# Performance work log

Measured on AMD Instinct MI355X. Metric: run time of the kernel, lower is better.

## Reference

```python
import jax, jax.numpy as jnp
import numpy as np

B, N, D = 2, 1024, 512
H, DH = 8, 64
HD = H * DH
FF = 2048
DEPTH = 4
SCALE = DH ** -0.5


def layer_norm(x, g, b, eps=1e-5):
    m = jnp.mean(x, axis=-1, keepdims=True)
    v = jnp.mean((x - m) ** 2, axis=-1, keepdims=True)
    return (x - m) / jnp.sqrt(v + eps) * g + b


def rel_shift(x):
    # x: (i, j, b, h) -> Transformer-XL relative shift via pad/reshape/slice
    i, j = x.shape[0], x.shape[1]
    zp = jnp.zeros((i, 1) + x.shape[2:], x.dtype)
    xp = jnp.concatenate([zp, x], axis=1).reshape((j + 1, i) + x.shape[2:])
    return xp[1:].reshape(x.shape)


def setup_inputs() -> dict:
    key = jax.random.key(0)
    ks = jax.random.split(key, 20)
    s = 0.02
    inp = {
        'x':   jax.random.normal(ks[0], (B, N, D), jnp.float32),
        'r_t': jax.random.normal(ks[1], (B, N, D), jnp.float32),
        'r_c': jax.random.normal(ks[2], (B, N, D), jnp.float32),
        'r_p': jax.random.normal(ks[3], (B, N, D), jnp.float32),
        'bias_pf': jax.random.normal(ks[4], (H, DH), jnp.float32) * s,
        'ln1_g': jnp.ones((DEPTH, D), jnp.float32),
        'ln1_b': jnp.zeros((DEPTH, D), jnp.float32),
        'w_qkv': jax.random.normal(ks[5], (DEPTH, D, 3 * HD), jnp.float32) * s,
        'w_out': jax.random.normal(ks[6], (DEPTH, HD, D), jnp.float32) * s,
        'b_out': jnp.zeros((DEPTH, D), jnp.float32),
        'w_kt': jax.random.normal(ks[7], (DEPTH, D, HD), jnp.float32) * s,
        'w_kc': jax.random.normal(ks[8], (DEPTH, D, HD), jnp.float32) * s,
        'w_kp': jax.random.normal(ks[9], (DEPTH, D, HD), jnp.float32) * s,
        'ln2_g': jnp.ones((DEPTH, D), jnp.float32),
        'ln2_b': jnp.zeros((DEPTH, D), jnp.float32),
        'w_ff1': jax.random.normal(ks[10], (DEPTH, D, FF), jnp.float32) * s,
        'b_ff1': jnp.zeros((DEPTH, FF), jnp.float32),
        'w_ff2': jax.random.normal(ks[11], (DEPTH, FF, D), jnp.float32) * s,
        'b_ff2': jnp.zeros((DEPTH, D), jnp.float32),
    }
    return inp


def _to_nbhd(t, b, n):
    # (b, n, h*d) -> (n, b, h, d)
    return t.reshape(b, n, H, DH).transpose(1, 0, 2, 3)


def reference(x, r_t, r_c, r_p, bias_pf, ln1_g, ln1_b, w_qkv, w_out, b_out,
              w_kt, w_kc, w_kp, ln2_g, ln2_b, w_ff1, b_ff1, w_ff2, b_ff2):
    b, n, _ = x.shape
    attn_last = None
    for l in range(DEPTH):
        xn = layer_norm(x, ln1_g[l], ln1_b[l])
        qkv = xn @ w_qkv[l]  # (b, n, 3*HD)
        q, k, v = jnp.split(qkv, 3, axis=-1)
        q = _to_nbhd(q, b, n) + bias_pf  # Ex_Wq + bias_pf, (n,b,h,d)
        k = _to_nbhd(k, b, n)
        v = _to_nbhd(v, b, n)
        wt = _to_nbhd(r_t @ w_kt[l], b, n)
        wc = _to_nbhd(r_c @ w_kc[l], b, n)
        wp = _to_nbhd(r_p @ w_kp[l], b, n)
        AC = jnp.einsum('ibhd,jbhd->ijbh', q, k)
        BD = (rel_shift(jnp.einsum('ibhd,jbhd->ijbh', q, wt))
              + rel_shift(jnp.einsum('ibhd,jbhd->ijbh', q, wc))
              + rel_shift(jnp.einsum('ibhd,jbhd->ijbh', q, wp))) * (1.0 / 3.0)
        dots = (AC + BD) * SCALE
        # NOTE: source uses nn.Softmax(dim=-1) on (i,j,b,h), i.e. over heads.
        attn = jax.nn.softmax(dots, axis=-1)
        out = jnp.einsum('ijbh,jbhd->ibhd', attn, v)
        out = out.transpose(1, 0, 2, 3).reshape(b, n, HD)
        x = out @ w_out[l] + b_out[l] + x
        xn2 = layer_norm(x, ln2_g[l], ln2_b[l])
        h1 = jax.nn.gelu(xn2 @ w_ff1[l] + b_ff1[l], approximate=False)
        x = h1 @ w_ff2[l] + b_ff2[l] + x
        attn_last = attn
    # attention rearranged 'q k b h -> b h q k'
    return x, attn_last.transpose(2, 3, 0, 1)
```

## Files before the change

### kernel.cpp

```cpp
#include <hip/hip_runtime.h>
#include <hip/hip_bf16.h>


using bf16 = __hip_bfloat16;
typedef __attribute__((ext_vector_type(8))) short short8;
typedef __attribute__((ext_vector_type(4))) float float4v;
typedef __attribute__((ext_vector_type(2))) unsigned int uint2v;

__device__ __forceinline__ float ldsel(const void* p, long long i, bool isbf) {
    return isbf ? __bfloat162float(((const bf16*)p)[i]) : ((const float*)p)[i];
}
__device__ __forceinline__ float bf2f(short u) {
    return __uint_as_float(((unsigned)(unsigned short)u) << 16);
}
__device__ __forceinline__ short f2bf(float f) {
    bf16 h = __float2bfloat16(f);
    return *reinterpret_cast<short*>(&h);
}

__global__ void detect_kernel(const unsigned int* __restrict__ g, int* __restrict__ flag) {
    if (threadIdx.x == 0) flag[0] = ((g[0] & 0xFFFFu) != 0u) ? 1 : 0;
}

__global__ __launch_bounds__(256) void input_prep(
    const void* __restrict__ x_in, const void* __restrict__ r0,
    const void* __restrict__ r1, const void* __restrict__ r2,
    float* __restrict__ xbuf, bf16* __restrict__ rcat,
    const int* __restrict__ flagp) {
    bool bf = flagp[0] != 0;
    int y = blockIdx.y;
    int i = blockIdx.x * 256 + threadIdx.x;
    if (y == 0) {
        long long b = (long long)i * 8;
        if (bf) {
            short8 v = *(const short8*)((const bf16*)x_in + b);
            float4v o0, o1;
            #pragma unroll
            for (int j = 0; j < 4; ++j) { o0[j] = bf2f(v[j]); o1[j] = bf2f(v[4 + j]); }
            *(float4v*)(xbuf + b) = o0;
            *(float4v*)(xbuf + b + 4) = o1;
        } else {
            float4v a0 = *(const float4v*)((const float*)x_in + b);
            float4v a1 = *(const float4v*)((const float*)x_in + b + 4);
            *(float4v*)(xbuf + b) = a0;
            *(float4v*)(xbuf + b + 4) = a1;
        }
    } else {
        int s = y - 1;
        const void* src = (s == 0) ? r0 : ((s == 1) ? r1 : r2);
        int m = i >> 6, k8 = (i & 63) * 8;
        long long b = (long long)m * 512 + k8;
        short8 v;
        if (bf) {
            v = *(const short8*)((const bf16*)src + b);
        } else {
            float4v a0 = *(const float4v*)((const float*)src + b);
            float4v a1 = *(const float4v*)((const float*)src + b + 4);
            #pragma unroll
            for (int j = 0; j < 4; ++j) { v[j] = f2bf(a0[j]); v[4 + j] = f2bf(a1[j]); }
        }
        *(short8*)(rcat + (size_t)m * 1536 + s * 512 + k8) = v;
    }
}

__global__ __launch_bounds__(256) void outputs_kernel(
    const float* __restrict__ xbuf, const bf16* __restrict__ attn,
    void* __restrict__ out, const int* __restrict__ flagp) {
    bool bf = flagp[0] != 0;
    int bid = blockIdx.x;
    if (bid < 512) {
        long long b = ((long long)bid * 256 + threadIdx.x) * 8;
        float4v a0 = *(const float4v*)(xbuf + b);
        float4v a1 = *(const float4v*)(xbuf + b + 4);
        if (bf) {
            short8 v;
            #pragma unroll
            for (int j = 0; j < 4; ++j) { v[j] = f2bf(a0[j]); v[4 + j] = f2bf(a1[j]); }
            *(short8*)((bf16*)out + b) = v;
        } else {
            *(float4v*)((float*)out + b) = a0;
            *(float4v*)((float*)out + b + 4) = a1;
        }
    } else {
        long long e = ((long long)(bid - 512) * 256 + threadIdx.x) * 8;
        short8 v = *(const short8*)(attn + e);
        if (bf) {
            *(short8*)((bf16*)out + 1048576 + e) = v;
        } else {
            float4v o0, o1;
            #pragma unroll
            for (int j = 0; j < 4; ++j) { o0[j] = bf2f(v[j]); o1[j] = bf2f(v[4 + j]); }
            float* op = (float*)out + 1048576 + e;
            *(float4v*)op = o0;
            *(float4v*)(op + 4) = o1;
        }
    }
}

__global__ __launch_bounds__(256) void prep_weights(
    const void* __restrict__ s0, const void* __restrict__ s1, const void* __restrict__ s2,
    const void* __restrict__ s3, const void* __restrict__ s4, const void* __restrict__ s5,
    const void* __restrict__ s6, const void* __restrict__ g1, const void* __restrict__ g2,
    bf16* __restrict__ arena, const int* __restrict__ flagp) {
    const bool bf = flagp[0] != 0;
    const int bid = blockIdx.x;
    const int l = bid / 960;
    const int rem = bid - l * 960;
    const int LW = 3932160;
    const int L = l * LW;

    int j, tile, tx, ldi, ldo;
    long long ioff;
    int dstoff;
    if (rem < 192)      { j = 0; tile = rem;                tx = 24; ldi = 1536; ldo = 512;
                          ioff = (long long)l * 786432;  dstoff = L; }
    else if (rem < 448) { j = 1 + ((rem - 192) >> 6); tile = (rem - 192) & 63; tx = 8; ldi = 512;
                          ioff = (long long)l * 262144;
                          if (j <= 3) { ldo = 1536; dstoff = L + 786432 + (j - 1) * 512; }
                          else        { ldo = 512;  dstoff = L + 1572864; } }
    else if (rem < 704) { j = 5; tile = rem - 448;          tx = 32; ldi = 2048; ldo = 512;
                          ioff = (long long)l * 1048576; dstoff = L + 1835008; }
    else                { j = 6; tile = rem - 704;          tx = 8;  ldi = 512;  ldo = 2048;
                          ioff = (long long)l * 1048576; dstoff = L + 2883584; }
    const void* in = (j == 0) ? s0 : (j == 1) ? s1 : (j == 2) ? s2 :
                     (j == 3) ? s3 : (j == 4) ? s4 : (j == 5) ? s5 : s6;
    const int gsel = (j == 0) ? 1 : ((j == 5) ? 2 : 0);
    bf16* out = arena + dstoff;
    const int bx = tile % tx, by = tile / tx;
    const int n0 = bx * 64, k0 = by * 64;
    const int tid = threadIdx.x;

    __shared__ bf16 t[64][72];

    if (bf) {
        const bf16* inb = (const bf16*)in + ioff;
        #pragma unroll
        for (int p = 0; p < 2; ++p) {
            int e = tid + p * 256;
            int r = e >> 3, c = (e & 7) * 8;
            *(uint4*)&t[r][c] = *(const uint4*)(inb + (size_t)(k0 + r) * ldi + n0 + c);
        }
    } else {
        const float* inf = (const float*)in + ioff;
        #pragma unroll
        for (int p = 0; p < 4; ++p) {
            int e = tid + p * 256;
            int r = e >> 4, c = (e & 15) * 4;
            float4v v = *(const float4v*)(inf + (size_t)(k0 + r) * ldi + n0 + c);
            union { bf16 h[4]; uint2v u; } w;
            #pragma unroll
            for (int q = 0; q < 4; ++q) w.h[q] = __float2bfloat16(v[q]);
            *reinterpret_cast<uint2v*>(&t[r][c]) = w.u;
        }
    }
    __syncthreads();
    #pragma unroll
    for (int p = 0; p < 2; ++p) {
        int e = tid + p * 256;
        int r = e >> 3, c = (e & 7) * 8;
        union { short8 s; uint4 u; } o;
        if (gsel) {
            const void* gp = (gsel == 1) ? g1 : g2;
            const long long go = (long long)l * 512 + k0 + c;
            #pragma unroll
            for (int q = 0; q < 8; ++q) {
                float gv = ldsel(gp, go + q, bf);
                o.s[q] = f2bf(bf2f(*reinterpret_cast<const short*>(&t[c + q][r])) * gv);
            }
        } else {
            #pragma unroll
            for (int q = 0; q < 8; ++q)
                o.s[q] = *reinterpret_cast<const short*>(&t[c + q][r]);
        }
        *(uint4*)(out + (size_t)(n0 + r) * ldo + k0 + c) = o.u;
    }
}

__global__ __launch_bounds__(256) void bvec_kernel(
    const void* __restrict__ w_qkv, const void* __restrict__ w_ff1,
    const void* __restrict__ ln1_b, const void* __restrict__ ln2_b,
    const void* __restrict__ bias_pf, const void* __restrict__ b_ff1,
    float* __restrict__ bBq, float* __restrict__ bBf,
    const int* __restrict__ flagp) {
    bool bf = flagp[0] != 0;
    int bid = blockIdx.x;
    int l = bid / 14, r = bid - l * 14;
    int tid = threadIdx.x;
    __shared__ float bs[512];

    const void* W; long long woff; int ldw, n0; const void* beta; float* out;
    if (r < 6) { W = w_qkv; woff = (long long)l * 786432;  ldw = 1536; n0 = r * 256;
                 beta = ln1_b; out = bBq + l * 1536; }
    else       { W = w_ff1; woff = (long long)l * 1048576; ldw = 2048; n0 = (r - 6) * 256;
                 beta = ln2_b; out = bBf + l * 2048; }
    long long boff = (long long)l * 512;
    bs[tid]       = ldsel(beta, boff + tid, bf);
    bs[tid + 256] = ldsel(beta, boff + tid + 256, bf);
    __syncthreads();
    float acc = 0.f;
    #pragma unroll 8
    for (int k = 0; k < 512; ++k)
        acc += bs[k] * ldsel(W, woff + (long long)k * ldw + n0 + tid, bf);
    int n = n0 + tid;
    if (r < 6) { if (n < 512) acc += ldsel(bias_pf, n, bf); }
    else       { acc += ldsel(b_ff1, (long long)l * 2048 + n, bf); }
    out[n] = acc;
}

__global__ __launch_bounds__(256) void ln_stats(const float* __restrict__ x,
                                                float2* __restrict__ st) {
    int row = blockIdx.x;
    const float* xr = x + (size_t)row * 512;
    int tid = threadIdx.x;
    float v0 = xr[tid], v1 = xr[tid + 256];
    float s = v0 + v1, q = v0 * v0 + v1 * v1;
    #pragma unroll
    for (int off = 32; off; off >>= 1) {
        s += __shfl_down(s, off);
        q += __shfl_down(q, off);
    }
    __shared__ float ls[4], lq[4];
    int wid = tid >> 6, lane = tid & 63;
    if (lane == 0) { ls[wid] = s; lq[wid] = q; }
    __syncthreads();
    if (tid == 0) {
        float ts = ls[0] + ls[1] + ls[2] + ls[3];
        float tq = lq[0] + lq[1] + lq[2] + lq[3];
        float m = ts * (1.f / 512.f);
        float var = tq * (1.f / 512.f) - m * m;
        st[row] = make_float2(m, rsqrtf(var + 1e-5f));
    }
}

template<int EPI>
__global__ __launch_bounds__(256) void mgemm64(
    const bf16* __restrict__ A, int lda, long long sAb, long long sAh,
    const bf16* __restrict__ B, int ldb, long long sBb, long long sBh,
    void* __restrict__ Cv, int ldc, long long sCb, long long sCh,
    int K,
    const void* __restrict__ bias, long long biasoff,
    float* __restrict__ resid,
    const int* __restrict__ flagp) {
    const bool flg = flagp[0] != 0;
    const int tid = threadIdx.x;
    const int lane = tid & 63, wave = tid >> 6;
    const int m0 = blockIdx.y * 64, n0 = blockIdx.x * 64;
    const int zb = (int)(blockIdx.z >> 3), zh = (int)(blockIdx.z & 7);
    A += (size_t)zb * sAb + (size_t)zh * sAh;
    B += (size_t)zb * sBb + (size_t)zh * sBh;

    __shared__ bf16 As[64][40];
    __shared__ bf16 Bs[64][40];

    const int ar = tid >> 2, ak = (tid & 3) * 8;
    const bf16* Ap = A + (size_t)(m0 + ar) * lda + ak;
    const bf16* Bp = B + (size_t)(n0 + ar) * ldb + ak;

    const int wm = (wave >> 1) * 32, wn = (wave & 1) * 32;
    const int fr = lane & 15, fq = lane >> 4;

    float4v acc[2][2] = {};

    uint4 a0 = *(const uint4*)Ap;
    uint4 b0 = *(const uint4*)Bp;

    for (int k0 = 0; k0 < K; k0 += 32) {
        __syncthreads();
        *(uint4*)&As[ar][ak] = a0;
        *(uint4*)&Bs[ar][ak] = b0;
        if (k0 + 32 < K) {
            a0 = *(const uint4*)(Ap + k0 + 32);
            b0 = *(const uint4*)(Bp + k0 + 32);
        }
        __syncthreads();
        union { uint4 u; short8 s; } ua[2], ub[2];
        #pragma unroll
        for (int i = 0; i < 2; ++i) ua[i].u = *(const uint4*)&As[wm + i * 16 + fr][fq * 8];
        #pragma unroll
        for (int j = 0; j < 2; ++j) ub[j].u = *(const uint4*)&Bs[wn + j * 16 + fr][fq * 8];
        #pragma unroll
        for (int i = 0; i < 2; ++i)
            #pragma unroll
            for (int j = 0; j < 2; ++j)
                acc[i][j] = __builtin_amdgcn_mfma_f32_16x16x32_bf16(ua[i].s, ub[j].s, acc[i][j], 0, 0, 0);
    }

    const long long coff = (long long)zb * sCb + (long long)zh * sCh;
    #pragma unroll
    for (int i = 0; i < 2; ++i) {
        #pragma unroll
        for (int j = 0; j < 2; ++j) {
            #pragma unroll
            for (int r = 0; r < 4; ++r) {
                int m = m0 + wm + i * 16 + fq * 4 + r;
                int n = n0 + wn + j * 16 + fr;
                float v = acc[i][j][r];
                if (EPI == 2) {
                    float* C = (float*)Cv;
                    C[(size_t)m * ldc + n] = v + ldsel(bias, biasoff + n, flg) + resid[(size_t)m * ldc + n];
                } else if (EPI == 5) {
                    bf16* C = (bf16*)Cv + coff;
                    C[(size_t)m * ldc + n] = __float2bfloat16(v);
                }
            }
        }
    }
}

template<int EPI>
__global__ __launch_bounds__(256) void mgemm64f(
    const float* __restrict__ A, const float2* __restrict__ stats,
    const bf16* __restrict__ B, int ldb,
    void* __restrict__ Cv, int ldc,
    const float* __restrict__ bB,
    bf16* __restrict__ aux) {
    const int tid = threadIdx.x;
    const int lane = tid & 63, wave = tid >> 6;
    const int m0 = blockIdx.y * 64, n0 = blockIdx.x * 64;

    __shared__ bf16 As[64][40];
    __shared__ bf16 Bs[64][40];

    const int ar = tid >> 2, ak = (tid & 3) * 8;
    const float* Ap = A + (size_t)(m0 + ar) * 512 + ak;
    const bf16* Bp  = B + (size_t)(n0 + ar) * ldb + ak;
    const float2 st = stats[m0 + ar];

    const int wm = (wave >> 1) * 32, wn = (wave & 1) * 32;
    const int fr = lane & 15, fq = lane >> 4;

    float4v acc[2][2] = {};

    float4v af0 = *(const float4v*)Ap;
    float4v af1 = *(const float4v*)(Ap + 4);
    uint4 b0 = *(const uint4*)Bp;

    for (int k0 = 0; k0 < 512; k0 += 32) {
        __syncthreads();
        union { bf16 h[8]; uint4 u; } w;
        #pragma unroll
        for (int u = 0; u < 4; ++u) {
            w.h[u]     = __float2bfloat16((af0[u] - st.x) * st.y);
            w.h[4 + u] = __float2bfloat16((af1[u] - st.x) * st.y);
        }
        *(uint4*)&As[ar][ak] = w.u;
        *(uint4*)&Bs[ar][ak] = b0;
        if (k0 + 32 < 512) {
            af0 = *(const float4v*)(Ap + k0 + 32);
            af1 = *(const float4v*)(Ap + k0 + 36);
            b0  = *(const uint4*)(Bp + k0 + 32);
        }
        __syncthreads();
        union { uint4 u; short8 s; } ua[2], ub[2];
        #pragma unroll
        for (int i = 0; i < 2; ++i) ua[i].u = *(const uint4*)&As[wm + i * 16 + fr][fq * 8];
        #pragma unroll
        for (int j = 0; j < 2; ++j) ub[j].u = *(const uint4*)&Bs[wn + j * 16 + fr][fq * 8];
        #pragma unroll
        for (int i = 0; i < 2; ++i)
            #pragma unroll
            for (int j = 0; j < 2; ++j)
                acc[i][j] = __builtin_amdgcn_mfma_f32_16x16x32_bf16(ua[i].s, ub[j].s, acc[i][j], 0, 0, 0);
    }

    #pragma unroll
    for (int i = 0; i < 2; ++i) {
        #pragma unroll
        for (int j = 0; j < 2; ++j) {
            #pragma unroll
            for (int r = 0; r < 4; ++r) {
                int m = m0 + wm + i * 16 + fq * 4 + r;
                int n = n0 + wn + j * 16 + fr;
                float v = acc[i][j][r] + bB[n];
                if (EPI == 1) {
                    bf16* C = (bf16*)Cv;
                    if (n < 1024) {
                        C[(size_t)m * ldc + n] = __float2bfloat16(v);
                    } else {
                        int h = (n >> 6) & 7, d = n & 63, ii = m & 1023, bb = m >> 10;
                        aux[(size_t)(bb * 8 + h) * 65536 + (size_t)d * 1024 + ii] = __float2bfloat16(v);
                    }
                } else if (EPI == 3) {
                    bf16* C = (bf16*)Cv;
                    C[(size_t)m * ldc + n] = __float2bfloat16(0.5f * v * (1.f + erff(v * 0.70710678118f)));
                }
            }
        }
    }
}

__global__ __launch_bounds__(512) void bd_kernel(
    const bf16* __restrict__ qkvb, const bf16* __restrict__ wsum,
    bf16* __restrict__ Scb) {
    const int tid = threadIdx.x;
    const int lane = tid & 63, wave = tid >> 6;
    const int n0 = blockIdx.x * 64, m0 = blockIdx.y * 64, b = blockIdx.z;

    __shared__ bf16 Qs[64][72];
    __shared__ bf16 Ws[64][72];

    const int r0 = tid >> 3, c0 = (tid & 7) * 8;
    const bf16* Qp = qkvb + (size_t)(b * 1024 + m0 + r0) * 1536 + c0;
    const bf16* Wp = wsum + (size_t)(b * 1024 + n0 + r0) * 512 + c0;

    const int wm = (wave >> 2) * 32, wn = (wave & 3) * 16;
    const int fr = lane & 15, fq = lane >> 4;

    float4v acc[8][2] = {};

    uint4 qreg = *(const uint4*)Qp;
    uint4 wreg = *(const uint4*)Wp;

    for (int h = 0; h < 8; ++h) {
        __syncthreads();
        *(uint4*)&Qs[r0][c0] = qreg;
        *(uint4*)&Ws[r0][c0] = wreg;
        if (h < 7) {
            qreg = *(const uint4*)(Qp + (h + 1) * 64);
            wreg = *(const uint4*)(Wp + (h + 1) * 64);
        }
        __syncthreads();
        #pragma unroll
        for (int ks = 0; ks < 2; ++ks) {
            union { uint4 u; short8 s; } ua[2], ub;
            #pragma unroll
            for (int i = 0; i < 2; ++i) ua[i].u = *(const uint4*)&Qs[wm + i * 16 + fr][fq * 8 + ks * 32];
            ub.u = *(const uint4*)&Ws[wn + fr][fq * 8 + ks * 32];
            #pragma unroll
            for (int i = 0; i < 2; ++i)
                acc[h][i] = __builtin_amdgcn_mfma_f32_16x16x32_bf16(ua[i].s, ub.s, acc[h][i], 0, 0, 0);
        }
    }

    const size_t pb = (size_t)b * 8388608;
    #pragma unroll
    for (int i = 0; i < 2; ++i) {
        #pragma unroll
        for (int r = 0; r < 4; ++r) {
            int m = m0 + wm + i * 16 + fq * 4 + r;
            int n = n0 + wn + fr;
            int t = m * 1025 + n + 1;
            if (t >= 1024) {
                short8 v;
                #pragma unroll
                for (int h = 0; h < 8; ++h) v[h] = f2bf(acc[h][i][r] * (1.f / 3.f));
                *(short8*)(Scb + pb + (size_t)(t - 1024) * 8) = v;
            }
        }
    }
}

__global__ __launch_bounds__(512) void scores_kernel(
    const bf16* __restrict__ qkvb, const bf16* __restrict__ Scb,
    bf16* __restrict__ attn) {
    const int tid = threadIdx.x;
    const int lane = tid & 63, wave = tid >> 6;
    const int j0 = blockIdx.x * 64, i0 = blockIdx.y * 64, b = blockIdx.z;

    __shared__ bf16 Qs[64][72];
    __shared__ bf16 Ks[64][72];

    const int r0 = tid >> 3, c0 = (tid & 7) * 8;
    const bf16* Qp = qkvb + (size_t)(b * 1024 + i0 + r0) * 1536 + c0;
    const bf16* Kp = qkvb + (size_t)(b * 1024 + j0 + r0) * 1536 + 512 + c0;

    const int wm = (wave >> 2) * 32, wn = (wave & 3) * 16;
    const int fr = lane & 15, fq = lane >> 4;

    float4v acc[8][2] = {};

    uint4 qreg = *(const uint4*)Qp;
    uint4 kreg = *(const uint4*)Kp;

    for (int h = 0; h < 8; ++h) {
        __syncthreads();
        *(uint4*)&Qs[r0][c0] = qreg;
        *(uint4*)&Ks[r0][c0] = kreg;
        if (h < 7) {
            qreg = *(const uint4*)(Qp + (h + 1) * 64);
            kreg = *(const uint4*)(Kp + (h + 1) * 64);
        }
        __syncthreads();
        #pragma unroll
        for (int ks = 0; ks < 2; ++ks) {
            union { uint4 u; short8 s; } ua[2], ub;
            #pragma unroll
            for (int i = 0; i < 2; ++i) ua[i].u = *(const uint4*)&Qs[wm + i * 16 + fr][fq * 8 + ks * 32];
            ub.u = *(const uint4*)&Ks[wn + fr][fq * 8 + ks * 32];
            #pragma unroll
            for (int i = 0; i < 2; ++i)
                acc[h][i] = __builtin_amdgcn_mfma_f32_16x16x32_bf16(ua[i].s, ub.s, acc[h][i], 0, 0, 0);
        }
    }

    short8 bdv[8];
    float mxs[8], invs[8];
    const size_t pb = (size_t)b * 8388608;
    #pragma unroll
    for (int i = 0; i < 2; ++i) {
        #pragma unroll
        for (int r = 0; r < 4; ++r) {
            const int e = i * 4 + r;
            int gi = i0 + wm + i * 16 + fq * 4 + r;
            int gj = j0 + wn + fr;
            bdv[e] = *(const short8*)(Scb + pb + ((size_t)gi * 1024 + gj) * 8);
            bool diag = (gj == gi + 1);
            float dv[8];
            float mx = -3.4e38f;
            #pragma unroll
            for (int h = 0; h < 8; ++h) {
                float bd = diag ? 0.f : bf2f(bdv[e][h]);
                dv[h] = (acc[h][i][r] + bd) * 0.125f;
                mx = fmaxf(mx, dv[h]);
            }
            float s = 0.f;
            #pragma unroll
            for (int h = 0; h < 8; ++h) s += __expf(dv[h] - mx);
            mxs[e] = mx; invs[e] = 1.f / s;
        }
    }

    const size_t ab = (size_t)b * 8388608;
    const int orow = tid >> 3, ocol = (tid & 7) * 8;
    #pragma unroll
    for (int h = 0; h < 8; ++h) {
        __syncthreads();
        #pragma unroll
        for (int i = 0; i < 2; ++i) {
            #pragma unroll
            for (int r = 0; r < 4; ++r) {
                const int e = i * 4 + r;
                int gil = wm + i * 16 + fq * 4 + r;
                int gjl = wn + fr;
                int gi = i0 + gil, gj = j0 + gjl;
                float bd = (gj == gi + 1) ? 0.f : bf2f(bdv[e][h]);
                float a = __expf((acc[h][i][r] + bd) * 0.125f - mxs[e]) * invs[e];
                Qs[gil][gjl] = __float2bfloat16(a);
            }
        }
        __syncthreads();
        *(uint4*)(attn + ab + (size_t)h * 1048576 + (size_t)(i0 + orow) * 1024 + j0 + ocol)
            = *(const uint4*)&Qs[orow][ocol];
    }
}

extern "C" void kernel_launch(void* const* d_in, const int* in_sizes, int n_in,
                              void* d_out, int out_size, void* d_ws, size_t ws_size,
                              hipStream_t stream) {
    (void)in_sizes; (void)n_in; (void)out_size; (void)ws_size;
    const void* x_in    = d_in[0];
    const void* r_t     = d_in[1];
    const void* r_c     = d_in[2];
    const void* r_p     = d_in[3];
    const void* bias_pf = d_in[4];
    const void* ln1_g   = d_in[5];
    const void* ln1_b   = d_in[6];
    const void* w_qkv   = d_in[7];
    const void* w_outw  = d_in[8];
    const void* b_out   = d_in[9];
    const void* w_kt    = d_in[10];
    const void* w_kc    = d_in[11];
    const void* w_kp    = d_in[12];
    const void* ln2_g   = d_in[13];
    const void* ln2_b   = d_in[14];
    const void* w_ff1   = d_in[15];
    const void* b_ff1   = d_in[16];
    const void* w_ff2   = d_in[17];
    const void* b_ff2   = d_in[18];

    float* xbuf  = (float*)d_ws;
    bf16* base16 = (bf16*)(xbuf + 1048576);
    bf16* Scb   = base16;
    bf16* h1    = base16;
    bf16* attn  = base16 + 16777216;
    bf16* xnb   = attn + 16777216;
    bf16* qkvb  = xnb + 1048576;
    bf16* vT    = qkvb + 3145728;
    bf16* wsum4 = vT + 1048576;
    bf16* rcat  = wsum4 + 4194304;
    bf16* arena = rcat + 3145728;
    int*   flagp = (int*)(arena + 15728640);
    float* bBq4  = (float*)(flagp + 16);
    float* bBf4  = bBq4 + 6144;
    float2* stats = (float2*)(bBf4 + 8192);

    const int LW = 3932160;
    const int WCAT_O = 786432, OUT_O = 1572864, FF1_O = 1835008, FF2_O = 2883584;
    const int QKV_O = 0;

    dim3 blk(256), blk8(512);

    detect_kernel<<<1, 64, 0, stream>>>((const unsigned int*)ln1_g, flagp);
    input_prep<<<dim3(512, 4), blk, 0, stream>>>(x_in, r_t, r_c, r_p, xbuf, rcat, flagp);

    prep_weights<<<3840, blk, 0, stream>>>(
        w_qkv, w_kt, w_kc, w_kp, w_outw, w_ff1, w_ff2, ln1_g, ln2_g, arena, flagp);

    bvec_kernel<<<56, blk, 0, stream>>>(
        w_qkv, w_ff1, ln1_b, ln2_b, bias_pf, b_ff1, bBq4, bBf4, flagp);

    mgemm64<5><<<dim3(8, 32, 4), blk, 0, stream>>>(
        rcat, 1536, 0, 0, arena + WCAT_O, 1536, 0, LW,
        wsum4, 512, 0, 1048576, 1536, nullptr, 0, nullptr, flagp);

    for (int l = 0; l < 4; ++l) {
        const bf16* qkvT  = arena + l * LW + QKV_O;
        const bf16* outT  = arena + l * LW + OUT_O;
        const bf16* ff1T  = arena + l * LW + FF1_O;
        const bf16* ff2T  = arena + l * LW + FF2_O;
        const bf16* wsum  = wsum4 + (size_t)l * 1048576;

        ln_stats<<<2048, blk, 0, stream>>>(xbuf, stats);
        mgemm64f<1><<<dim3(24, 32), blk, 0, stream>>>(
            xbuf, stats, qkvT, 512, qkvb, 1536, bBq4 + l * 1536, vT);
        bd_kernel<<<dim3(16, 16, 2), blk8, 0, stream>>>(qkvb, wsum, Scb);
        scores_kernel<<<dim3(16, 16, 2), blk8, 0, stream>>>(qkvb, Scb, attn);
        mgemm64<5><<<dim3(1, 16, 16), blk, 0, stream>>>(
            attn, 1024, 8388608, 1048576, vT, 1024, 524288, 65536,
            xnb, 512, 524288, 64, 1024, nullptr, 0, nullptr, flagp);
        mgemm64<2><<<dim3(8, 32, 1), blk, 0, stream>>>(
            xnb, 512, 0, 0, outT, 512, 0, 0,
            xbuf, 512, 0, 0, 512, b_out, (long long)l * 512, xbuf, flagp);
        ln_stats<<<2048, blk, 0, stream>>>(xbuf, stats);
        mgemm64f<3><<<dim3(32, 32), blk, 0, stream>>>(
            xbuf, stats, ff1T, 512, h1, 2048, bBf4 + l * 2048, nullptr);
        mgemm64<2><<<dim3(8, 32, 1), blk, 0, stream>>>(
            h1, 2048, 0, 0, ff2T, 2048, 0, 0,
            xbuf, 512, 0, 0, 2048, b_ff2, (long long)l * 512, xbuf, flagp);
    }

    outputs_kernel<<<8704, blk, 0, stream>>>(xbuf, attn, d_out, flagp);
}
```

Baseline: 733.7 us.

## Fuse layernorm statistics into residual GEMM epilogues and fold bias-vector precompute into weight prep

The separate ln_stats kernels are removed. Row sums and sums of squares are now built in the residual-add GEMM epilogues and in input_prep, using shuffles and atomics into per-stage stat buffers that a new init kernel zeroes. The LN-fused GEMMs derive mean and rstd from those sums. The bvec kernel is also folded into prep_weights, which computes the beta·W bias with atomics. This cuts 8 launches and their extra passes over x, at the cost of atomic traffic and a less stable E[x²]-mean² variance.

```diff
diff --git a/kernel.cpp b/kernel.cpp
--- a/kernel.cpp
+++ b/kernel.cpp
@@ -22,29 +22,53 @@
     if (threadIdx.x == 0) flag[0] = ((g[0] & 0xFFFFu) != 0u) ? 1 : 0;
 }
 
+__global__ __launch_bounds__(256) void init_kernel(
+    const void* __restrict__ bias_pf, const void* __restrict__ b_ff1,
+    float* __restrict__ bBq, float* __restrict__ bBf, float* __restrict__ stz,
+    const int* __restrict__ flagp) {
+    bool bf = flagp[0] != 0;
+    int idx = blockIdx.x * 256 + threadIdx.x;
+    if (idx < 36864) { stz[idx] = 0.f; return; }
+    int j = idx - 36864;
+    if (j < 6144) {
+        int n = j % 1536;
+        bBq[j] = (n < 512) ? ldsel(bias_pf, n, bf) : 0.f;
+    } else if (j < 14336) {
+        int jj = j - 6144;
+        bBf[jj] = ldsel(b_ff1, jj, bf);
+    }
+}
+
 __global__ __launch_bounds__(256) void input_prep(
     const void* __restrict__ x_in, const void* __restrict__ r0,
     const void* __restrict__ r1, const void* __restrict__ r2,
     float* __restrict__ xbuf, bf16* __restrict__ rcat,
-    const int* __restrict__ flagp) {
+    float2* __restrict__ st0, const int* __restrict__ flagp) {
     bool bf = flagp[0] != 0;
     int y = blockIdx.y;
     int i = blockIdx.x * 256 + threadIdx.x;
     if (y == 0) {
         long long b = (long long)i * 8;
+        float4v o0, o1;
         if (bf) {
             short8 v = *(const short8*)((const bf16*)x_in + b);
-            float4v o0, o1;
             #pragma unroll
             for (int j = 0; j < 4; ++j) { o0[j] = bf2f(v[j]); o1[j] = bf2f(v[4 + j]); }
-            *(float4v*)(xbuf + b) = o0;
-            *(float4v*)(xbuf + b + 4) = o1;
         } else {
-            float4v a0 = *(const float4v*)((const float*)x_in + b);
-            float4v a1 = *(const float4v*)((const float*)x_in + b + 4);
-            *(float4v*)(xbuf + b) = a0;
-            *(float4v*)(xbuf + b + 4) = a1;
-        }
+            o0 = *(const float4v*)((const float*)x_in + b);
+            o1 = *(const float4v*)((const float*)x_in + b + 4);
+        }
+        *(float4v*)(xbuf + b) = o0;
+        *(float4v*)(xbuf + b + 4) = o1;
+        float s = 0.f, q = 0.f;
+        #pragma unroll
+        for (int j = 0; j < 4; ++j) {
+            s += o0[j] + o1[j];
+            q += o0[j] * o0[j] + o1[j] * o1[j];
+        }
+        #pragma unroll
+        for (int o = 32; o; o >>= 1) { s += __shfl_xor(s, o); q += __shfl_xor(q, o); }
+        if ((threadIdx.x & 63) == 0) st0[i >> 6] = make_float2(s, q);
     } else {
         int s = y - 1;
         const void* src = (s == 0) ? r0 : ((s == 1) ? r1 : r2);
@@ -101,6 +125,8 @@
     const void* __restrict__ s0, const void* __restrict__ s1, const void* __restrict__ s2,
     const void* __restrict__ s3, const void* __restrict__ s4, const void* __restrict__ s5,
     const void* __restrict__ s6, const void* __restrict__ g1, const void* __restrict__ g2,
+    const void* __restrict__ b1, const void* __restrict__ b2,
+    float* __restrict__ bBq, float* __restrict__ bBf,
     bf16* __restrict__ arena, const int* __restrict__ flagp) {
     const bool bf = flagp[0] != 0;
     const int bid = blockIdx.x;
@@ -131,6 +157,7 @@
     const int tid = threadIdx.x;
 
     __shared__ bf16 t[64][72];
+    __shared__ float red[4][64];
 
     if (bf) {
         const bf16* inb = (const bf16*)in + ioff;
@@ -174,61 +201,22 @@
         }
         *(uint4*)(out + (size_t)(n0 + r) * ldo + k0 + c) = o.u;
     }
-}
-
-__global__ __launch_bounds__(256) void bvec_kernel(
-    const void* __restrict__ w_qkv, const void* __restrict__ w_ff1,
-    const void* __restrict__ ln1_b, const void* __restrict__ ln2_b,
-    const void* __restrict__ bias_pf, const void* __restrict__ b_ff1,
-    float* __restrict__ bBq, float* __restrict__ bBf,
-    const int* __restrict__ flagp) {
-    bool bf = flagp[0] != 0;
-    int bid = blockIdx.x;
-    int l = bid / 14, r = bid - l * 14;
-    int tid = threadIdx.x;
-    __shared__ float bs[512];
-
-    const void* W; long long woff; int ldw, n0; const void* beta; float* out;
-    if (r < 6) { W = w_qkv; woff = (long long)l * 786432;  ldw = 1536; n0 = r * 256;
-                 beta = ln1_b; out = bBq + l * 1536; }
-    else       { W = w_ff1; woff = (long long)l * 1048576; ldw = 2048; n0 = (r - 6) * 256;
-                 beta = ln2_b; out = bBf + l * 2048; }
-    long long boff = (long long)l * 512;
-    bs[tid]       = ldsel(beta, boff + tid, bf);
-    bs[tid + 256] = ldsel(beta, boff + tid + 256, bf);
-    __syncthreads();
-    float acc = 0.f;
-    #pragma unroll 8
-    for (int k = 0; k < 512; ++k)
-        acc += bs[k] * ldsel(W, woff + (long long)k * ldw + n0 + tid, bf);
-    int n = n0 + tid;
-    if (r < 6) { if (n < 512) acc += ldsel(bias_pf, n, bf); }
-    else       { acc += ldsel(b_ff1, (long long)l * 2048 + n, bf); }
-    out[n] = acc;
-}
-
-__global__ __launch_bounds__(256) void ln_stats(const float* __restrict__ x,
-                                                float2* __restrict__ st) {
-    int row = blockIdx.x;
-    const float* xr = x + (size_t)row * 512;
-    int tid = threadIdx.x;
-    float v0 = xr[tid], v1 = xr[tid + 256];
-    float s = v0 + v1, q = v0 * v0 + v1 * v1;
-    #pragma unroll
-    for (int off = 32; off; off >>= 1) {
-        s += __shfl_down(s, off);
-        q += __shfl_down(q, off);
-    }
-    __shared__ float ls[4], lq[4];
-    int wid = tid >> 6, lane = tid & 63;
-    if (lane == 0) { ls[wid] = s; lq[wid] = q; }
-    __syncthreads();
-    if (tid == 0) {
-        float ts = ls[0] + ls[1] + ls[2] + ls[3];
-        float tq = lq[0] + lq[1] + lq[2] + lq[3];
-        float m = ts * (1.f / 512.f);
-        float var = tq * (1.f / 512.f) - m * m;
-        st[row] = make_float2(m, rsqrtf(var + 1e-5f));
+
+    if (gsel) {
+        const void* bp = (gsel == 1) ? b1 : b2;
+        float* bout = (gsel == 1) ? (bBq + l * 1536 + n0) : (bBf + l * 2048 + n0);
+        const int c = tid & 63, seg = tid >> 6;
+        float partial = 0.f;
+        #pragma unroll
+        for (int q = 0; q < 16; ++q) {
+            int r = seg * 16 + q;
+            partial += ldsel(bp, (long long)l * 512 + k0 + r, bf)
+                     * bf2f(*reinterpret_cast<const short*>(&t[r][c]));
+        }
+        red[seg][c] = partial;
+        __syncthreads();
+        if (seg == 0)
+            atomicAdd(&bout[c], red[0][c] + red[1][c] + red[2][c] + red[3][c]);
     }
 }
 
@@ -240,6 +228,7 @@
     int K,
     const void* __restrict__ bias, long long biasoff,
     float* __restrict__ resid,
+    float2* __restrict__ stout,
     const int* __restrict__ flagp) {
     const bool flg = flagp[0] != 0;
     const int tid = threadIdx.x;
@@ -285,25 +274,43 @@
                 acc[i][j] = __builtin_amdgcn_mfma_f32_16x16x32_bf16(ua[i].s, ub[j].s, acc[i][j], 0, 0, 0);
     }
 
-    const long long coff = (long long)zb * sCb + (long long)zh * sCh;
-    #pragma unroll
-    for (int i = 0; i < 2; ++i) {
-        #pragma unroll
-        for (int j = 0; j < 2; ++j) {
+    if (EPI == 2) {
+        float* C = (float*)Cv;
+        #pragma unroll
+        for (int i = 0; i < 2; ++i) {
             #pragma unroll
             for (int r = 0; r < 4; ++r) {
                 int m = m0 + wm + i * 16 + fq * 4 + r;
-                int n = n0 + wn + j * 16 + fr;
-                float v = acc[i][j][r];
-                if (EPI == 2) {
-                    float* C = (float*)Cv;
-                    C[(size_t)m * ldc + n] = v + ldsel(bias, biasoff + n, flg) + resid[(size_t)m * ldc + n];
-                } else if (EPI == 5) {
-                    bf16* C = (bf16*)Cv + coff;
-                    C[(size_t)m * ldc + n] = __float2bfloat16(v);
+                float s = 0.f, q = 0.f;
+                #pragma unroll
+                for (int j = 0; j < 2; ++j) {
+                    int n = n0 + wn + j * 16 + fr;
+                    float v = acc[i][j][r] + ldsel(bias, biasoff + n, flg)
+                            + resid[(size_t)m * ldc + n];
+                    C[(size_t)m * ldc + n] = v;
+                    s += v; q += v * v;
+                }
+                #pragma unroll
+                for (int o = 8; o; o >>= 1) { s += __shfl_xor(s, o); q += __shfl_xor(q, o); }
+                if (fr == 0) {
+                    atomicAdd(&stout[m].x, s);
+                    atomicAdd(&stout[m].y, q);
                 }
             }
         }
+    } else {
+        const long long coff = (long long)zb * sCb + (long long)zh * sCh;
+        bf16* C = (bf16*)Cv + coff;
+        #pragma unroll
+        for (int i = 0; i < 2; ++i)
+            #pragma unroll
+            for (int j = 0; j < 2; ++j)
+                #pragma unroll
+                for (int r = 0; r < 4; ++r) {
+                    int m = m0 + wm + i * 16 + fq * 4 + r;
+                    int n = n0 + wn + j * 16 + fr;
+                    C[(size_t)m * ldc + n] = __float2bfloat16(acc[i][j][r]);
+                }
     }
 }
 
@@ -324,7 +331,9 @@
     const int ar = tid >> 2, ak = (tid & 3) * 8;
     const float* Ap = A + (size_t)(m0 + ar) * 512 + ak;
     const bf16* Bp  = B + (size_t)(n0 + ar) * ldb + ak;
-    const float2 st = stats[m0 + ar];
+    const float2 sq = stats[m0 + ar];
+    const float mean = sq.x * (1.f / 512.f);
+    const float rstd = rsqrtf(sq.y * (1.f / 512.f) - mean * mean + 1e-5f);
 
     const int wm = (wave >> 1) * 32, wn = (wave & 1) * 32;
     const int fr = lane & 15, fq = lane >> 4;
@@ -340,8 +349,8 @@
         union { bf16 h[8]; uint4 u; } w;
         #pragma unroll
         for (int u = 0; u < 4; ++u) {
-            w.h[u]     = __float2bfloat16((af0[u] - st.x) * st.y);
-            w.h[4 + u] = __float2bfloat16((af1[u] - st.x) * st.y);
+            w.h[u]     = __float2bfloat16((af0[u] - mean) * rstd);
+            w.h[4 + u] = __float2bfloat16((af1[u] - mean) * rstd);
         }
         *(uint4*)&As[ar][ak] = w.u;
         *(uint4*)&Bs[ar][ak] = b0;
@@ -582,7 +591,7 @@
     int*   flagp = (int*)(arena + 15728640);
     float* bBq4  = (float*)(flagp + 16);
     float* bBf4  = bBq4 + 6144;
-    float2* stats = (float2*)(bBf4 + 8192);
+    float2* st8  = (float2*)(bBf4 + 8192);
 
     const int LW = 3932160;
     const int WCAT_O = 786432, OUT_O = 1572864, FF1_O = 1835008, FF2_O = 2883584;
@@ -591,17 +600,16 @@
     dim3 blk(256), blk8(512);
 
     detect_kernel<<<1, 64, 0, stream>>>((const unsigned int*)ln1_g, flagp);
-    input_prep<<<dim3(512, 4), blk, 0, stream>>>(x_in, r_t, r_c, r_p, xbuf, rcat, flagp);
+    init_kernel<<<200, blk, 0, stream>>>(bias_pf, b_ff1, bBq4, bBf4, (float*)st8, flagp);
+    input_prep<<<dim3(512, 4), blk, 0, stream>>>(x_in, r_t, r_c, r_p, xbuf, rcat, st8, flagp);
 
     prep_weights<<<3840, blk, 0, stream>>>(
-        w_qkv, w_kt, w_kc, w_kp, w_outw, w_ff1, w_ff2, ln1_g, ln2_g, arena, flagp);
-
-    bvec_kernel<<<56, blk, 0, stream>>>(
-        w_qkv, w_ff1, ln1_b, ln2_b, bias_pf, b_ff1, bBq4, bBf4, flagp);
+        w_qkv, w_kt, w_kc, w_kp, w_outw, w_ff1, w_ff2, ln1_g, ln2_g,
+        ln1_b, ln2_b, bBq4, bBf4, arena, flagp);
 
     mgemm64<5><<<dim3(8, 32, 4), blk, 0, stream>>>(
         rcat, 1536, 0, 0, arena + WCAT_O, 1536, 0, LW,
-        wsum4, 512, 0, 1048576, 1536, nullptr, 0, nullptr, flagp);
+        wsum4, 512, 0, 1048576, 1536, nullptr, 0, nullptr, nullptr, flagp);
 
     for (int l = 0; l < 4; ++l) {
         const bf16* qkvT  = arena + l * LW + QKV_O;
@@ -610,23 +618,25 @@
         const bf16* ff2T  = arena + l * LW + FF2_O;
         const bf16* wsum  = wsum4 + (size_t)l * 1048576;
 
-        ln_stats<<<2048, blk, 0, stream>>>(xbuf, stats);
         mgemm64f<1><<<dim3(24, 32), blk, 0, stream>>>(
-            xbuf, stats, qkvT, 512, qkvb, 1536, bBq4 + l * 1536, vT);
+            xbuf, st8 + (size_t)(2 * l) * 2048, qkvT, 512, qkvb, 1536,
+            bBq4 + l * 1536, vT);
         bd_kernel<<<dim3(16, 16, 2), blk8, 0, stream>>>(qkvb, wsum, Scb);
         scores_kernel<<<dim3(16, 16, 2), blk8, 0, stream>>>(qkvb, Scb, attn);
         mgemm64<5><<<dim3(1, 16, 16), blk, 0, stream>>>(
             attn, 1024, 8388608, 1048576, vT, 1024, 524288, 65536,
-            xnb, 512, 524288, 64, 1024, nullptr, 0, nullptr, flagp);
+            xnb, 512, 524288, 64, 1024, nullptr, 0, nullptr, nullptr, flagp);
         mgemm64<2><<<dim3(8, 32, 1), blk, 0, stream>>>(
             xnb, 512, 0, 0, outT, 512, 0, 0,
-            xbuf, 512, 0, 0, 512, b_out, (long long)l * 512, xbuf, flagp);
-        ln_stats<<<2048, blk, 0, stream>>>(xbuf, stats);
+            xbuf, 512, 0, 0, 512, b_out, (long long)l * 512, xbuf,
+            st8 + (size_t)(2 * l + 1) * 2048, flagp);
         mgemm64f<3><<<dim3(32, 32), blk, 0, stream>>>(
-            xbuf, stats, ff1T, 512, h1, 2048, bBf4 + l * 2048, nullptr);
+            xbuf, st8 + (size_t)(2 * l + 1) * 2048, ff1T, 512, h1, 2048,
+            bBf4 + l * 2048, nullptr);
         mgemm64<2><<<dim3(8, 32, 1), blk, 0, stream>>>(
             h1, 2048, 0, 0, ff2T, 2048, 0, 0,
-            xbuf, 512, 0, 0, 2048, b_ff2, (long long)l * 512, xbuf, flagp);
+            xbuf, 512, 0, 0, 2048, b_ff2, (long long)l * 512, xbuf,
+            st8 + (size_t)(2 * l + 2) * 2048, flagp);
     }
 
     outputs_kernel<<<8704, blk, 0, stream>>>(xbuf, attn, d_out, flagp);
```

Measured after the change: 683.4 us. 1.07x faster.
